# Performance work log

Measured on AMD Instinct MI355X. Metric: run time of the kernel, lower is better.

Reference implementation:

```python
import jax, jax.numpy as jnp
import numpy as np

B = 8192
ND, NS, NF = 13, 26, 39          # dense feats, sparse feats, seq_len
E, H, HD = 64, 8, 8              # embed_dim, heads, head_dim
L = 4                            # num_layers
FF = 4 * E                       # 256 mlp hidden
HID = 256                        # output head hidden
VD, VS = 50, 50000               # vocab sizes
SCALE = HD ** -0.5
EPS = 1e-5


def setup_inputs() -> dict:
    key = jax.random.key(0)
    ks = iter(jax.random.split(key, 32))
    n = lambda shape, s=0.02: jax.random.normal(next(ks), shape, jnp.float32) * s
    inp = {
        "dense_feats": jax.random.randint(next(ks), (B, ND), 0, VD),
        "sparse_feats": jax.random.randint(next(ks), (B, NS), 0, VS),
        "dense_emb": n((ND, VD, E)),
        "sparse_emb": n((NS, VS, E)),
        # per-layer params stacked on leading L axis (for lax.scan)
        "wq": n((L, E, E)), "bq": jnp.zeros((L, E)),
        "wk": n((L, E, E)), "bk": jnp.zeros((L, E)),
        "wv": n((L, E, E)), "bv": jnp.zeros((L, E)),
        "wo": n((L, E, E)), "bo": jnp.zeros((L, E)),
        "ln1_g": jnp.ones((L, E)), "ln1_b": jnp.zeros((L, E)),
        "ln2_g": jnp.ones((L, E)), "ln2_b": jnp.zeros((L, E)),
        "mlp_w1": n((L, E, FF)), "mlp_b1": jnp.zeros((L, FF)),
        "mlp_w2": n((L, FF, E)), "mlp_b2": jnp.zeros((L, E)),
        "out_w1": n((E * NF, HID)), "out_b1": jnp.zeros((HID,)),
        "out_w2": n((HID, 1)), "out_b2": jnp.zeros((1,)),
    }
    return inp


def _layernorm(x, g, b):
    m = jnp.mean(x, -1, keepdims=True)
    v = jnp.var(x, -1, keepdims=True)
    return (x - m) * jax.lax.rsqrt(v + EPS) * g + b


def _block(x, p):
    (wq, bq, wk, bk, wv, bv, wo, bo, g1, be1, g2, be2, w1, b1, w2, b2) = p
    h = _layernorm(x, g1, be1)
    bsz = h.shape[0]
    q = (h @ wq + bq).reshape(bsz, NF, H, HD)
    k = (h @ wk + bk).reshape(bsz, NF, H, HD)
    v = (h @ wv + bv).reshape(bsz, NF, H, HD)
    attn = jax.nn.sigmoid(jnp.einsum('bqhd,bkhd->bhqk', q, k) * SCALE)
    o = jnp.einsum('bhqk,bkhd->bqhd', attn, v).reshape(bsz, NF, E)
    x = x + (o @ wo + bo)
    h2 = _layernorm(x, g2, be2)
    x = x + (jax.nn.gelu(h2 @ w1 + b1) @ w2 + b2)
    return x, None


def reference(dense_feats, sparse_feats, dense_emb, sparse_emb,
              wq, bq, wk, bk, wv, bv, wo, bo,
              ln1_g, ln1_b, ln2_g, ln2_b,
              mlp_w1, mlp_b1, mlp_w2, mlp_b2,
              out_w1, out_b1, out_w2, out_b2):
    # 39-way embedding gather -> [B, 39, E]
    de = dense_emb[jnp.arange(ND)[None, :], dense_feats]    # [B,13,E]
    se = sparse_emb[jnp.arange(NS)[None, :], sparse_feats]  # [B,26,E]
    x = jnp.concatenate([de, se], axis=1)
    params = (wq, bq, wk, bk, wv, bv, wo, bo,
              ln1_g, ln1_b, ln2_g, ln2_b, mlp_w1, mlp_b1, mlp_w2, mlp_b2)
    x, _ = jax.lax.scan(_block, x, params)
    flat = x.reshape(x.shape[0], -1)                        # [B, 39*E]
    h = jax.nn.relu(flat @ out_w1 + out_b1)
    return jax.nn.sigmoid(h @ out_w2 + out_b2)[:, 0]        # [B]
```

## Files before the change

### kernel.cpp

```cpp
#include <hip/hip_runtime.h>
#include <hip/hip_bf16.h>

#define NDENSE 13
#define NSPARSE 26
#define NFEAT 39
#define EDIM 64
#define NLAYER 4
#define FFDIM 256
#define VDN 50
#define VSN 50000
#define NSAMP 8192
#define LN_EPS 1e-5f

#define QSCL 0.5100697f
#define GC1 2.3022082f
#define GC2 0.10294324f

#define XST 72
#define QST 72
#define VST2 56
#define FST2 136

#define OFF_XB 0
#define OFF_QB 5760
#define OFF_KB 12672
#define OFF_VT 19584
#define SMEM_TOTAL 26752
#define OFF_FF OFF_QB
#define OFF_LNS OFF_VT

#define FLATX_ELEMS (8192L * NFEAT * EDIM)
#define PK_WKT 4096
#define PK_WVT 8192
#define PK_WOT 12288
#define PK_W1T 16384
#define PK_W2T 32768
#define PK_LAYER 49152
#define PK_OW1T 196608
#define PK_TOTAL 835584
#define FB_PER_LAYER 448

typedef __bf16 bf16x8 __attribute__((ext_vector_type(8)));
typedef __bf16 bf16x4 __attribute__((ext_vector_type(4)));
typedef float f32x4 __attribute__((ext_vector_type(4)));
typedef int int32x4 __attribute__((ext_vector_type(4)));

__device__ __forceinline__ f32x4 mfma16(bf16x8 a, bf16x8 b, f32x4 c) {
    return __builtin_amdgcn_mfma_f32_16x16x32_bf16(a, b, c, 0, 0, 0);
}

__device__ __forceinline__ float exp2_fast(float x) {
#if __has_builtin(__builtin_amdgcn_exp2f)
    return __builtin_amdgcn_exp2f(x);
#else
    return exp2f(x);
#endif
}
__device__ __forceinline__ float sigmoid2(float x) {
    return __builtin_amdgcn_rcpf(1.0f + exp2_fast(-x));
}
__device__ __forceinline__ float gelu_f(float x) {
    return x * sigmoid2(GC1 * x + GC2 * x * x * x);
}

__device__ __forceinline__ bf16x8 ldfrag(const __bf16* WT, int ld, int col, int k0) {
    return *(const bf16x8*)&WT[col * ld + k0];
}
__device__ __forceinline__ bf16x4 pk4(f32x4 v) {
    bf16x4 r; r[0]=(__bf16)v[0]; r[1]=(__bf16)v[1]; r[2]=(__bf16)v[2]; r[3]=(__bf16)v[3]; return r;
}
__device__ __forceinline__ int pk2(float a, float b) {
    unsigned short ua = __builtin_bit_cast(unsigned short, (__bf16)a);
    unsigned short ub = __builtin_bit_cast(unsigned short, (__bf16)b);
    return (int)(((unsigned)ub << 16) | (unsigned)ua);
}
__device__ __forceinline__ void rmw4(__bf16* p, f32x4 a) {
    bf16x4 o = *(bf16x4*)p;
    f32x4 n = { (float)o[0]+a[0], (float)o[1]+a[1], (float)o[2]+a[2], (float)o[3]+a[3] };
    *(bf16x4*)p = pk4(n);
}

__device__ __forceinline__ void norm_frag(const __bf16* xr, int g, bf16x8& a0, bf16x8& a1) {
    bf16x8 v0 = *(const bf16x8*)(xr + g * 8);
    bf16x8 v1 = *(const bf16x8*)(xr + 32 + g * 8);
    float x0[8], x1[8], s = 0.f, ss = 0.f;
    #pragma unroll
    for (int j = 0; j < 8; ++j) {
        x0[j] = (float)v0[j]; x1[j] = (float)v1[j];
        s += x0[j] + x1[j];
        ss += x0[j] * x0[j] + x1[j] * x1[j];
    }
    s += __shfl_xor(s, 16); ss += __shfl_xor(ss, 16);
    s += __shfl_xor(s, 32); ss += __shfl_xor(ss, 32);
    float mn = s * (1.0f / 64.0f);
    float rs = rsqrtf(ss * (1.0f / 64.0f) - mn * mn + LN_EPS);
    #pragma unroll
    for (int j = 0; j < 8; ++j) {
        a0[j] = (__bf16)((x0[j] - mn) * rs);
        a1[j] = (__bf16)((x1[j] - mn) * rs);
    }
}

__device__ __forceinline__ void qk_tile(const __bf16* Qb, const __bf16* Kb,
                                        int h, int kt, int g, int r16, int sp[3][2]) {
    bf16x8 kf = {};
    if (g == 0) kf = *(const bf16x8*)&Kb[(16*kt + r16) * QST + 8*h];
    #pragma unroll
    for (int qt = 0; qt < 3; ++qt) {
        bf16x8 qf = {};
        if (g == 0) qf = *(const bf16x8*)&Qb[(16*qt + r16) * QST + 8*h];
        f32x4 acc = {0.f, 0.f, 0.f, 0.f};
        acc = mfma16(kf, qf, acc);
        sp[qt][0] = pk2(sigmoid2(acc[0]), sigmoid2(acc[1]));
        sp[qt][1] = pk2(sigmoid2(acc[2]), sigmoid2(acc[3]));
    }
}

__global__ __launch_bounds__(256)
void pack_weights(const float* __restrict__ wq, const float* __restrict__ wk,
                  const float* __restrict__ wv, const float* __restrict__ wo,
                  const float* __restrict__ w1, const float* __restrict__ w2,
                  const float* __restrict__ ow1, const float* __restrict__ ln1g,
                  const float* __restrict__ ln2g, __bf16* __restrict__ pk)
{
    int idx = blockIdx.x * 256 + threadIdx.x;
    if (idx >= PK_TOTAL) return;
    float v;
    if (idx < PK_OW1T) {
        int l = idx / PK_LAYER, r = idx - l * PK_LAYER;
        const float* src; const float* gam = nullptr; int sh, N, off;
        if (r < PK_WKT)      { src = wq + l * 4096;  sh = 6; N = 64;  off = r;           gam = ln1g + l*64; }
        else if (r < PK_WVT) { src = wk + l * 4096;  sh = 6; N = 64;  off = r - PK_WKT;  gam = ln1g + l*64; }
        else if (r < PK_WOT) { src = wv + l * 4096;  sh = 6; N = 64;  off = r - PK_WVT;  gam = ln1g + l*64; }
        else if (r < PK_W1T) { src = wo + l * 4096;  sh = 6; N = 64;  off = r - PK_WOT; }
        else if (r < PK_W2T) { src = w1 + l * 16384; sh = 6; N = 256; off = r - PK_W1T;  gam = ln2g + l*64; }
        else                 { src = w2 + l * 16384; sh = 8; N = 64;  off = r - PK_W2T; }
        int col = off >> sh, k = off & ((1 << sh) - 1);
        v = src[k * N + col];
        if (gam) v *= gam[k];
    } else {
        int off = idx - PK_OW1T;
        int col = off / 2496, k = off - col * 2496;
        v = ow1[k * 256 + col];
    }
    pk[idx] = (__bf16)v;
}

__global__ __launch_bounds__(256)
void fold_bias(const float* __restrict__ wq, const float* __restrict__ wk,
               const float* __restrict__ wv, const float* __restrict__ w1,
               const float* __restrict__ bq, const float* __restrict__ bk,
               const float* __restrict__ bv, const float* __restrict__ b1,
               const float* __restrict__ ln1b, const float* __restrict__ ln2b,
               float* __restrict__ pkb)
{
    int idx = blockIdx.x * 256 + threadIdx.x;
    if (idx >= NLAYER * FB_PER_LAYER) return;
    int l = idx / FB_PER_LAYER, r = idx - l * FB_PER_LAYER;
    const float *W, *b, *beta; int col, N;
    if (r < 64)       { W = wq + l*4096;  b = bq + l*64;  beta = ln1b + l*64; col = r;       N = 64;  }
    else if (r < 128) { W = wk + l*4096;  b = bk + l*64;  beta = ln1b + l*64; col = r - 64;  N = 64;  }
    else if (r < 192) { W = wv + l*4096;  b = bv + l*64;  beta = ln1b + l*64; col = r - 128; N = 64;  }
    else              { W = w1 + l*16384; b = b1 + l*256; beta = ln2b + l*64; col = r - 192; N = 256; }
    float acc = b[col];
    for (int k = 0; k < 64; ++k) acc += beta[k] * W[k * N + col];
    pkb[idx] = acc;
}

__global__ __launch_bounds__(256, 4)
void hstu_fused(const int* __restrict__ dfeat, const int* __restrict__ sfeat,
                const float* __restrict__ demb, const float* __restrict__ semb,
                const float* __restrict__ bo, const float* __restrict__ b2,
                const __bf16* __restrict__ pk, const float* __restrict__ pkb,
                __bf16* __restrict__ flatX)
{
    __shared__ __align__(16) char smem[SMEM_TOTAL];
    __bf16* xb  = (__bf16*)(smem + OFF_XB);
    __bf16* Qb  = (__bf16*)(smem + OFF_QB);
    __bf16* Kb  = (__bf16*)(smem + OFF_KB);
    __bf16* Vt  = (__bf16*)(smem + OFF_VT);
    __bf16* ff  = (__bf16*)(smem + OFF_FF);
    __bf16* LNS = (__bf16*)(smem + OFF_LNS);

    const int tid = threadIdx.x;
    const int lane = tid & 63, w = tid >> 6;
    const int g = lane >> 4, r16 = lane & 15;
    const int oc = w;
    const int s0 = blockIdx.x;

    for (int r = w; r < 40; r += 4) {
        float val = 0.0f;
        if (r < NFEAT) {
            if (r < NDENSE) {
                int idx = dfeat[s0 * NDENSE + r];
                val = demb[(r * VDN + idx) * EDIM + lane];
            } else {
                int idx = sfeat[s0 * NSPARSE + (r - NDENSE)];
                val = semb[((long)(r - NDENSE) * VSN + idx) * EDIM + lane];
            }
        }
        xb[r * XST + lane] = (__bf16)val;
    }
    __syncthreads();

    for (int lay = 0; lay < NLAYER; ++lay) {
        const __bf16* wqT = pk + lay * PK_LAYER;
        const __bf16* wkT = wqT + PK_WKT;
        const __bf16* wvT = wqT + PK_WVT;
        const __bf16* woT = wqT + PK_WOT;
        const __bf16* w1T = wqT + PK_W1T;
        const __bf16* w2T = wqT + PK_W2T;
        const float* fb   = pkb + lay * FB_PER_LAYER;
        const float* bo_l = bo + lay * EDIM;
        const float* b2_l = b2 + lay * EDIM;

        {
            bf16x8 lnB[3][2];
            #pragma unroll
            for (int tt = 0; tt < 3; ++tt) {
                int q48 = 16 * tt + r16;
                int xr = q48 > 39 ? 39 : q48;
                norm_frag(&xb[xr * XST], g, lnB[tt][0], lnB[tt][1]);
            }

            const __bf16* Wm[3] = { wqT, wkT, wvT };
            #pragma unroll
            for (int m = 0; m < 3; ++m) {
                bf16x8 A0 = ldfrag(Wm[m], EDIM, 16 * oc + r16, 8 * g);
                bf16x8 A1 = ldfrag(Wm[m], EDIM, 16 * oc + r16, 32 + 8 * g);
                f32x4 bi4 = *(const f32x4*)&fb[m * 64 + 16 * oc + 4 * g];
                #pragma unroll
                for (int tt = 0; tt < 3; ++tt) {
                    f32x4 acc = bi4;
                    acc = mfma16(A0, lnB[tt][0], acc);
                    acc = mfma16(A1, lnB[tt][1], acc);
                    int q48 = 16 * tt + r16;
                    if (m == 0) {
                        f32x4 sc = { acc[0]*QSCL, acc[1]*QSCL, acc[2]*QSCL, acc[3]*QSCL };
                        *(bf16x4*)&Qb[q48 * QST + 16 * oc + 4 * g] = pk4(sc);
                    } else if (m == 1) {
                        *(bf16x4*)&Kb[q48 * QST + 16 * oc + 4 * g] = pk4(acc);
                    } else {
                        bool vz = q48 >= 39;
                        #pragma unroll
                        for (int r = 0; r < 4; ++r)
                            Vt[(16 * oc + 4 * g + r) * VST2 + q48] =
                                vz ? (__bf16)0.0f : (__bf16)acc[r];
                    }
                }
            }
        }
        __syncthreads();

        {
            const int sAh[3] = {0,0,1}, sAt[3] = {0,2,1};
            const int sBh[3] = {0,1,1}, sBt[3] = {1,0,2};
            const int l0 = ((lane & 16) << 1) + r16;
            const int l1 = l0 + 16;
            const bool selA = (g < 2);
            f32x4 oacc[3];
            {
                f32x4 z = {0.f, 0.f, 0.f, 0.f};
                oacc[0] = z; oacc[1] = z; oacc[2] = z;
            }
            #pragma unroll
            for (int ks = 0; ks < 3; ++ks) {
                int spA[3][2], spB[3][2];
                qk_tile(Qb, Kb, 2*oc + sAh[ks], sAt[ks], g, r16, spA);
                qk_tile(Qb, Kb, 2*oc + sBh[ks], sBt[ks], g, r16, spB);

                int slot0 = 32 * ks + 8 * g;
                int side = slot0 >= 48 ? 1 : 0;
                int kk0 = slot0 - 48 * side;
                bf16x8 av = {};
                if (side == (r16 >> 3))
                    av = *(const bf16x8*)&Vt[(16 * oc + r16) * VST2 + kk0];
                #pragma unroll
                for (int qt = 0; qt < 3; ++qt) {
                    int a0 = spA[qt][0], a1 = spA[qt][1];
                    int b0 = spB[qt][0], b1 = spB[qt][1];
                    int va0 = __shfl(a0, l0), va1 = __shfl(a1, l0);
                    int va2 = __shfl(a0, l1), va3 = __shfl(a1, l1);
                    int vb0 = __shfl(b0, l0), vb1 = __shfl(b1, l0);
                    int vb2 = __shfl(b0, l1), vb3 = __shfl(b1, l1);
                    int32x4 bi = { selA ? va0 : vb0, selA ? va1 : vb1,
                                   selA ? va2 : vb2, selA ? va3 : vb3 };
                    oacc[qt] = mfma16(av, __builtin_bit_cast(bf16x8, bi), oacc[qt]);
                }
            }
            #pragma unroll
            for (int qt = 0; qt < 3; ++qt) {
                int q48 = 16 * qt + r16;
                *(bf16x4*)&Qb[q48 * QST + 16 * oc + 4 * g] = pk4(oacc[qt]);
            }
        }
        __syncthreads();

        {
            bf16x8 A0 = ldfrag(woT, EDIM, 16 * oc + r16, 8 * g);
            bf16x8 A1 = ldfrag(woT, EDIM, 16 * oc + r16, 32 + 8 * g);
            f32x4 bo4 = *(const f32x4*)&bo_l[16 * oc + 4 * g];
            #pragma unroll
            for (int tt = 0; tt < 3; ++tt) {
                bf16x8 B0 = *(const bf16x8*)&Qb[(16 * tt + r16) * QST + 8 * g];
                bf16x8 B1 = *(const bf16x8*)&Qb[(16 * tt + r16) * QST + 32 + 8 * g];
                f32x4 acc = bo4;
                acc = mfma16(A0, B0, acc);
                acc = mfma16(A1, B1, acc);
                int ql = 16 * tt + r16;
                if (ql <= 39)
                    rmw4(&xb[ql * XST + 16 * oc + 4 * g], acc);
            }
        }
        __syncthreads();

        for (int u = w; u < 12; u += 4) {
            int ql = 4 * u + g;
            int qlc = ql > 39 ? 39 : ql;
            bf16x4 v = *(const bf16x4*)&xb[qlc * XST + 4 * r16];
            float x0 = (float)v[0], x1 = (float)v[1], x2 = (float)v[2], x3 = (float)v[3];
            float s = x0 + x1 + x2 + x3;
            float ss = x0*x0 + x1*x1 + x2*x2 + x3*x3;
            s += __shfl_xor(s, 1);  ss += __shfl_xor(ss, 1);
            s += __shfl_xor(s, 2);  ss += __shfl_xor(ss, 2);
            s += __shfl_xor(s, 4);  ss += __shfl_xor(ss, 4);
            s += __shfl_xor(s, 8);  ss += __shfl_xor(ss, 8);
            float mn = s * (1.0f / 64.0f);
            float rs = rsqrtf(ss * (1.0f / 64.0f) - mn * mn + LN_EPS);
            f32x4 nv = { (x0 - mn) * rs, (x1 - mn) * rs,
                         (x2 - mn) * rs, (x3 - mn) * rs };
            *(bf16x4*)&LNS[ql * 72 + 4 * r16] = pk4(nv);
        }
        __syncthreads();

        {
            bf16x8 upB[3][2];
            #pragma unroll
            for (int tt = 0; tt < 3; ++tt) {
                upB[tt][0] = *(const bf16x8*)&LNS[(16 * tt + r16) * 72 + 8 * g];
                upB[tt][1] = *(const bf16x8*)&LNS[(16 * tt + r16) * 72 + 32 + 8 * g];
            }
            f32x4 acc2[3];
            acc2[0] = *(const f32x4*)&b2_l[16 * oc + 4 * g];
            acc2[1] = acc2[0]; acc2[2] = acc2[0];

            #pragma unroll
            for (int p2 = 0; p2 < 2; ++p2) {
                #pragma unroll
                for (int fi = 0; fi < 2; ++fi) {
                    int ftl = 2 * w + fi;
                    int ftg = 8 * p2 + ftl;
                    bf16x8 A0 = ldfrag(w1T, EDIM, 16 * ftg + r16, 8 * g);
                    bf16x8 A1 = ldfrag(w1T, EDIM, 16 * ftg + r16, 32 + 8 * g);
                    f32x4 b14 = *(const f32x4*)&fb[192 + 16 * ftg + 4 * g];
                    #pragma unroll
                    for (int tt = 0; tt < 3; ++tt) {
                        f32x4 acc = b14;
                        acc = mfma16(A0, upB[tt][0], acc);
                        acc = mfma16(A1, upB[tt][1], acc);
                        f32x4 gl = { gelu_f(acc[0]), gelu_f(acc[1]),
                                     gelu_f(acc[2]), gelu_f(acc[3]) };
                        *(bf16x4*)&ff[(16 * tt + r16) * FST2 + 16 * ftl + 4 * g] = pk4(gl);
                    }
                }
                __syncthreads();

                #pragma unroll
                for (int tt = 0; tt < 3; ++tt) {
                    #pragma unroll
                    for (int kf = 0; kf < 4; ++kf) {
                        bf16x8 Af = ldfrag(w2T, FFDIM, 16 * oc + r16,
                                           128 * p2 + 32 * kf + 8 * g);
                        bf16x8 Bf = *(const bf16x8*)&ff[(16 * tt + r16) * FST2
                                                        + 32 * kf + 8 * g];
                        acc2[tt] = mfma16(Af, Bf, acc2[tt]);
                    }
                }
                __syncthreads();
            }
            #pragma unroll
            for (int tt = 0; tt < 3; ++tt) {
                int ql = 16 * tt + r16;
                if (ql <= 39)
                    rmw4(&xb[ql * XST + 16 * oc + 4 * g], acc2[tt]);
            }
        }
        __syncthreads();
    }

    for (int r = w; r < NFEAT; r += 4)
        flatX[((long)s0 * NFEAT + r) * EDIM + lane] = xb[r * XST + lane];
}

#define FFSTH 264
__global__ __launch_bounds__(512)
void final_mlp(const __bf16* __restrict__ flatX, const __bf16* __restrict__ ow1T,
               const float* __restrict__ ob1, const float* __restrict__ ow2,
               const float* __restrict__ ob2, float* __restrict__ out)
{
    __shared__ __bf16 hbuf[32 * FFSTH];
    const int tid = threadIdx.x, lane = tid & 63, wave = tid >> 6;
    const int g = lane >> 4, r16 = lane & 15;
    const int m = wave & 1;
    const long base = (long)blockIdx.x * 32;
    const long arow = (base + m * 16 + r16) * (long)(NFEAT * EDIM);

    f32x4 acc[4];
    #pragma unroll
    for (int i = 0; i < 4; ++i) {
        int n = (wave >> 1) + i * 4;
        float bz = ob1[n * 16 + r16];
        f32x4 t = {bz, bz, bz, bz};
        acc[i] = t;
    }
    for (int kf = 0; kf < 78; ++kf) {
        bf16x8 af = *(const bf16x8*)&flatX[arow + kf * 32 + g * 8];
        #pragma unroll
        for (int i = 0; i < 4; ++i) {
            int n = (wave >> 1) + i * 4;
            bf16x8 bfr = ldfrag(ow1T, NFEAT * EDIM, n * 16 + r16, kf * 32 + g * 8);
            acc[i] = mfma16(af, bfr, acc[i]);
        }
    }
    #pragma unroll
    for (int i = 0; i < 4; ++i) {
        int n = (wave >> 1) + i * 4;
        #pragma unroll
        for (int r = 0; r < 4; ++r) {
            float h = acc[i][r];
            hbuf[(m * 16 + g * 4 + r) * FFSTH + n * 16 + r16] = (__bf16)(h > 0.f ? h : 0.f);
        }
    }
    __syncthreads();
    float w2v0 = ow2[lane], w2v1 = ow2[64 + lane], w2v2 = ow2[128 + lane], w2v3 = ow2[192 + lane];
    float bias2 = ob2[0];
    #pragma unroll
    for (int i = 0; i < 4; ++i) {
        int sm = wave * 4 + i;
        float part = (float)hbuf[sm * FFSTH + lane]       * w2v0
                   + (float)hbuf[sm * FFSTH + 64 + lane]  * w2v1
                   + (float)hbuf[sm * FFSTH + 128 + lane] * w2v2
                   + (float)hbuf[sm * FFSTH + 192 + lane] * w2v3;
        #pragma unroll
        for (int off = 32; off >= 1; off >>= 1) part += __shfl_xor(part, off);
        if (lane == 0) {
            float z = part + bias2;
            out[base + sm] = __builtin_amdgcn_rcpf(1.0f + __expf(-z));
        }
    }
}

extern "C" void kernel_launch(void* const* d_in, const int* in_sizes, int n_in,
                              void* d_out, int out_size, void* d_ws, size_t ws_size,
                              hipStream_t stream)
{
    const int*   dfeat = (const int*)d_in[0];
    const int*   sfeat = (const int*)d_in[1];
    const float* demb  = (const float*)d_in[2];
    const float* semb  = (const float*)d_in[3];
    const float* wq    = (const float*)d_in[4];
    const float* bq    = (const float*)d_in[5];
    const float* wk    = (const float*)d_in[6];
    const float* bk    = (const float*)d_in[7];
    const float* wv    = (const float*)d_in[8];
    const float* bv    = (const float*)d_in[9];
    const float* wo    = (const float*)d_in[10];
    const float* bo    = (const float*)d_in[11];
    const float* ln1g  = (const float*)d_in[12];
    const float* ln1b  = (const float*)d_in[13];
    const float* ln2g  = (const float*)d_in[14];
    const float* ln2b  = (const float*)d_in[15];
    const float* w1    = (const float*)d_in[16];
    const float* b1    = (const float*)d_in[17];
    const float* w2    = (const float*)d_in[18];
    const float* b2    = (const float*)d_in[19];
    const float* ow1   = (const float*)d_in[20];
    const float* ob1   = (const float*)d_in[21];
    const float* ow2   = (const float*)d_in[22];
    const float* ob2   = (const float*)d_in[23];

    __bf16* flatX = (__bf16*)d_ws;
    __bf16* pk    = ((__bf16*)d_ws) + FLATX_ELEMS;
    float*  pkb   = (float*)(pk + PK_TOTAL);
    float* out = (float*)d_out;

    pack_weights<<<(PK_TOTAL + 255) / 256, 256, 0, stream>>>(wq, wk, wv, wo, w1, w2,
                                                             ow1, ln1g, ln2g, pk);
    fold_bias<<<(NLAYER * FB_PER_LAYER + 255) / 256, 256, 0, stream>>>(
        wq, wk, wv, w1, bq, bk, bv, b1, ln1b, ln2b, pkb);
    hstu_fused<<<NSAMP, 256, 0, stream>>>(dfeat, sfeat, demb, semb,
                                          bo, b2, pk, pkb, flatX);
    final_mlp<<<NSAMP / 32, 512, 0, stream>>>(flatX, pk + PK_OW1T, ob1, ow2, ob2, out);
}
```

Measured before the change: 741.0 us.

## Stage sigmoid attention scores through swizzled LDS and fold Q scale into weights

Attention score tiles are now written to a per-wave, XOR-swizzled LDS staging area and read back as MFMA B fragments. This replaces the cross-lane shuffle and select sequence used before. Q/K fragments are preloaded into registers so the Q buffer region can be reused as that staging area, which adds extra barriers. The first layernorm now uses the cooperative LDS-based routine shared with the second, replacing per-fragment redundant normalization. The attention scale is folded into the packed Wq weights and biases, removing a per-element multiply.

```diff
diff --git a/kernel.cpp b/kernel.cpp
--- a/kernel.cpp
+++ b/kernel.cpp
@@ -43,7 +43,6 @@
 typedef __bf16 bf16x8 __attribute__((ext_vector_type(8)));
 typedef __bf16 bf16x4 __attribute__((ext_vector_type(4)));
 typedef float f32x4 __attribute__((ext_vector_type(4)));
-typedef int int32x4 __attribute__((ext_vector_type(4)));
 
 __device__ __forceinline__ f32x4 mfma16(bf16x8 a, bf16x8 b, f32x4 c) {
     return __builtin_amdgcn_mfma_f32_16x16x32_bf16(a, b, c, 0, 0, 0);
@@ -69,50 +68,30 @@
 __device__ __forceinline__ bf16x4 pk4(f32x4 v) {
     bf16x4 r; r[0]=(__bf16)v[0]; r[1]=(__bf16)v[1]; r[2]=(__bf16)v[2]; r[3]=(__bf16)v[3]; return r;
 }
-__device__ __forceinline__ int pk2(float a, float b) {
-    unsigned short ua = __builtin_bit_cast(unsigned short, (__bf16)a);
-    unsigned short ub = __builtin_bit_cast(unsigned short, (__bf16)b);
-    return (int)(((unsigned)ub << 16) | (unsigned)ua);
-}
 __device__ __forceinline__ void rmw4(__bf16* p, f32x4 a) {
     bf16x4 o = *(bf16x4*)p;
     f32x4 n = { (float)o[0]+a[0], (float)o[1]+a[1], (float)o[2]+a[2], (float)o[3]+a[3] };
     *(bf16x4*)p = pk4(n);
 }
 
-__device__ __forceinline__ void norm_frag(const __bf16* xr, int g, bf16x8& a0, bf16x8& a1) {
-    bf16x8 v0 = *(const bf16x8*)(xr + g * 8);
-    bf16x8 v1 = *(const bf16x8*)(xr + 32 + g * 8);
-    float x0[8], x1[8], s = 0.f, ss = 0.f;
-    #pragma unroll
-    for (int j = 0; j < 8; ++j) {
-        x0[j] = (float)v0[j]; x1[j] = (float)v1[j];
-        s += x0[j] + x1[j];
-        ss += x0[j] * x0[j] + x1[j] * x1[j];
-    }
-    s += __shfl_xor(s, 16); ss += __shfl_xor(ss, 16);
-    s += __shfl_xor(s, 32); ss += __shfl_xor(ss, 32);
-    float mn = s * (1.0f / 64.0f);
-    float rs = rsqrtf(ss * (1.0f / 64.0f) - mn * mn + LN_EPS);
-    #pragma unroll
-    for (int j = 0; j < 8; ++j) {
-        a0[j] = (__bf16)((x0[j] - mn) * rs);
-        a1[j] = (__bf16)((x1[j] - mn) * rs);
-    }
-}
-
-__device__ __forceinline__ void qk_tile(const __bf16* Qb, const __bf16* Kb,
-                                        int h, int kt, int g, int r16, int sp[3][2]) {
-    bf16x8 kf = {};
-    if (g == 0) kf = *(const bf16x8*)&Kb[(16*kt + r16) * QST + 8*h];
-    #pragma unroll
-    for (int qt = 0; qt < 3; ++qt) {
-        bf16x8 qf = {};
-        if (g == 0) qf = *(const bf16x8*)&Qb[(16*qt + r16) * QST + 8*h];
-        f32x4 acc = {0.f, 0.f, 0.f, 0.f};
-        acc = mfma16(kf, qf, acc);
-        sp[qt][0] = pk2(sigmoid2(acc[0]), sigmoid2(acc[1]));
-        sp[qt][1] = pk2(sigmoid2(acc[2]), sigmoid2(acc[3]));
+__device__ __forceinline__ void coop_ln(const __bf16* xb, __bf16* LNS,
+                                        int w, int g, int r16) {
+    for (int u = w; u < 12; u += 4) {
+        int ql = 4 * u + g;
+        int qlc = ql > 39 ? 39 : ql;
+        bf16x4 v = *(const bf16x4*)&xb[qlc * XST + 4 * r16];
+        float x0 = (float)v[0], x1 = (float)v[1], x2 = (float)v[2], x3 = (float)v[3];
+        float s = x0 + x1 + x2 + x3;
+        float ss = x0*x0 + x1*x1 + x2*x2 + x3*x3;
+        s += __shfl_xor(s, 1);  ss += __shfl_xor(ss, 1);
+        s += __shfl_xor(s, 2);  ss += __shfl_xor(ss, 2);
+        s += __shfl_xor(s, 4);  ss += __shfl_xor(ss, 4);
+        s += __shfl_xor(s, 8);  ss += __shfl_xor(ss, 8);
+        float mn = s * (1.0f / 64.0f);
+        float rs = rsqrtf(ss * (1.0f / 64.0f) - mn * mn + LN_EPS);
+        f32x4 nv = { (x0 - mn) * rs, (x1 - mn) * rs,
+                     (x2 - mn) * rs, (x3 - mn) * rs };
+        *(bf16x4*)&LNS[ql * 72 + 4 * r16] = pk4(nv);
     }
 }
 
@@ -129,14 +108,15 @@
     if (idx < PK_OW1T) {
         int l = idx / PK_LAYER, r = idx - l * PK_LAYER;
         const float* src; const float* gam = nullptr; int sh, N, off;
-        if (r < PK_WKT)      { src = wq + l * 4096;  sh = 6; N = 64;  off = r;           gam = ln1g + l*64; }
+        float extra = 1.0f;
+        if (r < PK_WKT)      { src = wq + l * 4096;  sh = 6; N = 64;  off = r;           gam = ln1g + l*64; extra = QSCL; }
         else if (r < PK_WVT) { src = wk + l * 4096;  sh = 6; N = 64;  off = r - PK_WKT;  gam = ln1g + l*64; }
         else if (r < PK_WOT) { src = wv + l * 4096;  sh = 6; N = 64;  off = r - PK_WVT;  gam = ln1g + l*64; }
         else if (r < PK_W1T) { src = wo + l * 4096;  sh = 6; N = 64;  off = r - PK_WOT; }
         else if (r < PK_W2T) { src = w1 + l * 16384; sh = 6; N = 256; off = r - PK_W1T;  gam = ln2g + l*64; }
         else                 { src = w2 + l * 16384; sh = 8; N = 64;  off = r - PK_W2T; }
         int col = off >> sh, k = off & ((1 << sh) - 1);
-        v = src[k * N + col];
+        v = src[k * N + col] * extra;
         if (gam) v *= gam[k];
     } else {
         int off = idx - PK_OW1T;
@@ -157,14 +137,14 @@
     int idx = blockIdx.x * 256 + threadIdx.x;
     if (idx >= NLAYER * FB_PER_LAYER) return;
     int l = idx / FB_PER_LAYER, r = idx - l * FB_PER_LAYER;
-    const float *W, *b, *beta; int col, N;
-    if (r < 64)       { W = wq + l*4096;  b = bq + l*64;  beta = ln1b + l*64; col = r;       N = 64;  }
+    const float *W, *b, *beta; int col, N; float extra = 1.0f;
+    if (r < 64)       { W = wq + l*4096;  b = bq + l*64;  beta = ln1b + l*64; col = r;       N = 64;  extra = QSCL; }
     else if (r < 128) { W = wk + l*4096;  b = bk + l*64;  beta = ln1b + l*64; col = r - 64;  N = 64;  }
     else if (r < 192) { W = wv + l*4096;  b = bv + l*64;  beta = ln1b + l*64; col = r - 128; N = 64;  }
     else              { W = w1 + l*16384; b = b1 + l*256; beta = ln2b + l*64; col = r - 192; N = 256; }
     float acc = b[col];
     for (int k = 0; k < 64; ++k) acc += beta[k] * W[k * N + col];
-    pkb[idx] = acc;
+    pkb[idx] = acc * extra;
 }
 
 __global__ __launch_bounds__(256, 4)
@@ -214,15 +194,18 @@
         const float* bo_l = bo + lay * EDIM;
         const float* b2_l = b2 + lay * EDIM;
 
+        coop_ln(xb, LNS, w, g, r16);
+        __syncthreads();
+
+        bf16x8 lnB[3][2];
+        #pragma unroll
+        for (int tt = 0; tt < 3; ++tt) {
+            lnB[tt][0] = *(const bf16x8*)&LNS[(16 * tt + r16) * 72 + 8 * g];
+            lnB[tt][1] = *(const bf16x8*)&LNS[(16 * tt + r16) * 72 + 32 + 8 * g];
+        }
+        __syncthreads();
+
         {
-            bf16x8 lnB[3][2];
-            #pragma unroll
-            for (int tt = 0; tt < 3; ++tt) {
-                int q48 = 16 * tt + r16;
-                int xr = q48 > 39 ? 39 : q48;
-                norm_frag(&xb[xr * XST], g, lnB[tt][0], lnB[tt][1]);
-            }
-
             const __bf16* Wm[3] = { wqT, wkT, wvT };
             #pragma unroll
             for (int m = 0; m < 3; ++m) {
@@ -236,8 +219,7 @@
                     acc = mfma16(A1, lnB[tt][1], acc);
                     int q48 = 16 * tt + r16;
                     if (m == 0) {
-                        f32x4 sc = { acc[0]*QSCL, acc[1]*QSCL, acc[2]*QSCL, acc[3]*QSCL };
-                        *(bf16x4*)&Qb[q48 * QST + 16 * oc + 4 * g] = pk4(sc);
+                        *(bf16x4*)&Qb[q48 * QST + 16 * oc + 4 * g] = pk4(acc);
                     } else if (m == 1) {
                         *(bf16x4*)&Kb[q48 * QST + 16 * oc + 4 * g] = pk4(acc);
                     } else {
@@ -253,11 +235,25 @@
         __syncthreads();
 
         {
+            bf16x8 qf[2][3], kf[2][3];
+            #pragma unroll
+            for (int hh = 0; hh < 2; ++hh) {
+                #pragma unroll
+                for (int t = 0; t < 3; ++t) {
+                    bf16x8 z = {};
+                    qf[hh][t] = z; kf[hh][t] = z;
+                    if (g == 0) {
+                        qf[hh][t] = *(const bf16x8*)&Qb[(16*t + r16) * QST + 8*(2*oc + hh)];
+                        kf[hh][t] = *(const bf16x8*)&Kb[(16*t + r16) * QST + 8*(2*oc + hh)];
+                    }
+                }
+            }
+            __syncthreads();
+
+            char* st = (char*)Qb + w * 3072;
+
             const int sAh[3] = {0,0,1}, sAt[3] = {0,2,1};
             const int sBh[3] = {0,1,1}, sBt[3] = {1,0,2};
-            const int l0 = ((lane & 16) << 1) + r16;
-            const int l1 = l0 + 16;
-            const bool selA = (g < 2);
             f32x4 oacc[3];
             {
                 f32x4 z = {0.f, 0.f, 0.f, 0.f};
@@ -265,10 +261,22 @@
             }
             #pragma unroll
             for (int ks = 0; ks < 3; ++ks) {
-                int spA[3][2], spB[3][2];
-                qk_tile(Qb, Kb, 2*oc + sAh[ks], sAt[ks], g, r16, spA);
-                qk_tile(Qb, Kb, 2*oc + sBh[ks], sBt[ks], g, r16, spB);
-
+                #pragma unroll
+                for (int ts = 0; ts < 2; ++ts) {
+                    int hh = ts ? sBh[ks] : sAh[ks];
+                    int kt = ts ? sBt[ks] : sAt[ks];
+                    #pragma unroll
+                    for (int qt = 0; qt < 3; ++qt) {
+                        f32x4 acc = {0.f, 0.f, 0.f, 0.f};
+                        acc = mfma16(kf[hh][kt], qf[hh][qt], acc);
+                        f32x4 sg = { sigmoid2(acc[0]), sigmoid2(acc[1]),
+                                     sigmoid2(acc[2]), sigmoid2(acc[3]) };
+                        int q = 16 * qt + r16;
+                        int blk = 2 * ts + (g >> 1);
+                        int off = q * 64 + ((blk ^ (q & 3)) << 4) + ((g & 1) << 3);
+                        *(bf16x4*)(st + off) = pk4(sg);
+                    }
+                }
                 int slot0 = 32 * ks + 8 * g;
                 int side = slot0 >= 48 ? 1 : 0;
                 int kk0 = slot0 - 48 * side;
@@ -277,17 +285,14 @@
                     av = *(const bf16x8*)&Vt[(16 * oc + r16) * VST2 + kk0];
                 #pragma unroll
                 for (int qt = 0; qt < 3; ++qt) {
-                    int a0 = spA[qt][0], a1 = spA[qt][1];
-                    int b0 = spB[qt][0], b1 = spB[qt][1];
-                    int va0 = __shfl(a0, l0), va1 = __shfl(a1, l0);
-                    int va2 = __shfl(a0, l1), va3 = __shfl(a1, l1);
-                    int vb0 = __shfl(b0, l0), vb1 = __shfl(b1, l0);
-                    int vb2 = __shfl(b0, l1), vb3 = __shfl(b1, l1);
-                    int32x4 bi = { selA ? va0 : vb0, selA ? va1 : vb1,
-                                   selA ? va2 : vb2, selA ? va3 : vb3 };
-                    oacc[qt] = mfma16(av, __builtin_bit_cast(bf16x8, bi), oacc[qt]);
-                }
-            }
+                    int q = 16 * qt + r16;
+                    int roff = q * 64 + ((g ^ (q & 3)) << 4);
+                    bf16x8 bfrag = *(const bf16x8*)(st + roff);
+                    oacc[qt] = mfma16(av, bfrag, oacc[qt]);
+                }
+            }
+            __syncthreads();
+
             #pragma unroll
             for (int qt = 0; qt < 3; ++qt) {
                 int q48 = 16 * qt + r16;
@@ -314,23 +319,7 @@
         }
         __syncthreads();
 
-        for (int u = w; u < 12; u += 4) {
-            int ql = 4 * u + g;
-            int qlc = ql > 39 ? 39 : ql;
-            bf16x4 v = *(const bf16x4*)&xb[qlc * XST + 4 * r16];
-            float x0 = (float)v[0], x1 = (float)v[1], x2 = (float)v[2], x3 = (float)v[3];
-            float s = x0 + x1 + x2 + x3;
-            float ss = x0*x0 + x1*x1 + x2*x2 + x3*x3;
-            s += __shfl_xor(s, 1);  ss += __shfl_xor(ss, 1);
-            s += __shfl_xor(s, 2);  ss += __shfl_xor(ss, 2);
-            s += __shfl_xor(s, 4);  ss += __shfl_xor(ss, 4);
-            s += __shfl_xor(s, 8);  ss += __shfl_xor(ss, 8);
-            float mn = s * (1.0f / 64.0f);
-            float rs = rsqrtf(ss * (1.0f / 64.0f) - mn * mn + LN_EPS);
-            f32x4 nv = { (x0 - mn) * rs, (x1 - mn) * rs,
-                         (x2 - mn) * rs, (x3 - mn) * rs };
-            *(bf16x4*)&LNS[ql * 72 + 4 * r16] = pk4(nv);
-        }
+        coop_ln(xb, LNS, w, g, r16);
         __syncthreads();
 
         {
@@ -368,11 +357,11 @@
                 #pragma unroll
                 for (int tt = 0; tt < 3; ++tt) {
                     #pragma unroll
-                    for (int kf = 0; kf < 4; ++kf) {
+                    for (int kf2 = 0; kf2 < 4; ++kf2) {
                         bf16x8 Af = ldfrag(w2T, FFDIM, 16 * oc + r16,
-                                           128 * p2 + 32 * kf + 8 * g);
+                                           128 * p2 + 32 * kf2 + 8 * g);
                         bf16x8 Bf = *(const bf16x8*)&ff[(16 * tt + r16) * FST2
-                                                        + 32 * kf + 8 * g];
+                                                        + 32 * kf2 + 8 * g];
                         acc2[tt] = mfma16(Af, Bf, acc2[tt]);
                     }
                 }
```

Result: faster. 688.8 us (-7.0%).
